# Performance work log

Hardware: AMD Instinct MI355X
Metric: run time of the kernel (lower is better)

The kernel has to match this reference:

```python
import jax, jax.numpy as jnp
import numpy as np

NUM_HEADS = 16
HEAD_DIM = 64
MAX_REL = 128
NEG_INF = -1e30


def setup_inputs() -> dict:
    key = jax.random.key(0)
    ks = jax.random.split(key, 5)
    B, L, D = 2, 2048, 1024
    x = jax.random.normal(ks[0], (B, L, D), dtype=jnp.float32)
    key_padding_mask = jnp.zeros((B, L), dtype=bool)  # True = padded
    Wqkv = jax.random.normal(ks[1], (D, 3 * D), dtype=jnp.float32) * (D ** -0.5)
    bqkv = jnp.zeros((3 * D,), dtype=jnp.float32)
    Wout = jax.random.normal(ks[2], (D, D), dtype=jnp.float32) * (D ** -0.5)
    bout = jnp.zeros((D,), dtype=jnp.float32)
    bias_table = jax.random.normal(ks[3], (2 * MAX_REL + 1, NUM_HEADS), dtype=jnp.float32) * 0.02
    return {"x": x, "key_padding_mask": key_padding_mask, "Wqkv": Wqkv,
            "bqkv": bqkv, "Wout": Wout, "bout": bout, "bias_table": bias_table}


def _rel_bias(bias_table, L):
    # relative position index: clamp(k - q, -MAX_REL, MAX_REL) + MAX_REL -> [L, L]
    rel = jnp.arange(L)[None, :] - jnp.arange(L)[:, None]
    idx = jnp.clip(rel, -MAX_REL, MAX_REL) + MAX_REL
    return bias_table[idx].transpose(2, 0, 1)  # [H, L, L]


def reference(x, key_padding_mask, Wqkv, bqkv, Wout, bout, bias_table):
    B, L, D = x.shape
    H, hd = NUM_HEADS, HEAD_DIM
    qkv = x @ Wqkv + bqkv                      # [B, L, 3D]
    q, k, v = jnp.split(qkv, 3, axis=-1)
    q = q.reshape(B, L, H, hd).transpose(0, 2, 1, 3)  # [B, H, L, hd]
    k = k.reshape(B, L, H, hd).transpose(0, 2, 1, 3)
    v = v.reshape(B, L, H, hd).transpose(0, 2, 1, 3)
    scores = jnp.einsum('bhqd,bhkd->bhqk', q, k) * (hd ** -0.5)
    scores = scores + _rel_bias(bias_table, L)[None]   # [B, H, L, L]
    scores = jnp.where(key_padding_mask[:, None, None, :], NEG_INF, scores)
    attn = jax.nn.softmax(scores, axis=-1)
    out = jnp.einsum('bhqk,bhkd->bhqd', attn, v)       # [B, H, L, hd]
    out = out.transpose(0, 2, 1, 3).reshape(B, L, D)
    return out @ Wout + bout
```

## Files before the change

kernel.cpp:

```cpp
#include <hip/hip_runtime.h>
#include <hip/hip_bf16.h>
#include <stdint.h>

#define LSEQ 2048
#define BATCH 2
#define DMODEL 1024
#define NH 16
#define HD 64

typedef __attribute__((ext_vector_type(8))) short bf16x8;
typedef __attribute__((ext_vector_type(4))) float f32x4;

__device__ __forceinline__ short f2bf(float f) {
  union { float f; uint32_t u; } v; v.f = f;
  uint32_t r = v.u + 0x8000u;
  return (short)(r >> 16);
}

__device__ __forceinline__ uint32_t pack_bf16(float lo, float hi) {
  union { float f; uint32_t u; } a, b; a.f = lo; b.f = hi;
  uint32_t al = (a.u + 0x8000u) >> 16;
  uint32_t bh = (b.u + 0x8000u) & 0xFFFF0000u;
  return al | bh;
}

__device__ __forceinline__ float exp2_fast(float x) {
#if __has_builtin(__builtin_amdgcn_exp2f)
  return __builtin_amdgcn_exp2f(x);
#else
  float r; asm("v_exp_f32 %0, %1" : "=v"(r) : "v"(x)); return r;
#endif
}

__device__ __forceinline__ void gll16(const void* g, void* l) {
  __builtin_amdgcn_global_load_lds(
      (const __attribute__((address_space(1))) void*)g,
      (__attribute__((address_space(3))) void*)l, 16, 0, 0);
}

__global__ void cvt_bf16(const float* __restrict__ in, short* __restrict__ out, int n) {
  int i = (blockIdx.x * blockDim.x + threadIdx.x) * 4;
  if (i < n) {
    float4 v = *(const float4*)(in + i);
    short4 o;
    o.x = f2bf(v.x); o.y = f2bf(v.y); o.z = f2bf(v.z); o.w = f2bf(v.w);
    *(short4*)(out + i) = o;
  }
}

__global__ void transpose_cvt(const float* __restrict__ in, short* __restrict__ out,
                              int K, int N) {
  __shared__ float tile[32][33];
  int kb = blockIdx.x * 32, nb = blockIdx.y * 32;
  int tx = threadIdx.x & 31, ty = threadIdx.x >> 5;
  #pragma unroll
  for (int i = ty; i < 32; i += 8)
    tile[i][tx] = in[(size_t)(kb + i) * N + nb + tx];
  __syncthreads();
  #pragma unroll
  for (int i = ty; i < 32; i += 8)
    out[(size_t)(nb + i) * K + kb + tx] = f2bf(tile[tx][i]);
}

template <int EPI>
__global__ __launch_bounds__(256, 2) void gemm_bt(
    const short* __restrict__ A, const short* __restrict__ Bt,
    const float* __restrict__ bias, float* __restrict__ outf,
    short* __restrict__ q_out, short* __restrict__ k_out, short* __restrict__ v_out) {
  constexpr int K = 1024, BK = 32;
  __shared__ short Als[128 * BK];
  __shared__ short Bls[128 * BK];
  const int tid = threadIdx.x;
  const int lane = tid & 63;
  const int m0 = blockIdx.x * 128;
  const int n0 = blockIdx.y * 128;
  const int wid = tid >> 6;
  const int wm = (wid >> 1) * 64, wn = (wid & 1) * 64;

  f32x4 acc[4][4] = {};

  for (int kt = 0; kt < K / BK; ++kt) {
    const int k0 = kt * BK;
    __syncthreads();
    #pragma unroll
    for (int inst = 0; inst < 2; ++inst) {
      int c = inst * 256 + tid;
      int row = c >> 2, cc = (c & 3) * 8;
      gll16(A + (size_t)(m0 + row) * K + k0 + cc, Als + c * 8);
      gll16(Bt + (size_t)(n0 + row) * K + k0 + cc, Bls + c * 8);
    }
    __syncthreads();
    bf16x8 af[4], bfv[4];
    #pragma unroll
    for (int m = 0; m < 4; ++m)
      af[m] = *(const bf16x8*)(Als + (wm + m * 16 + (lane & 15)) * BK + (lane >> 4) * 8);
    #pragma unroll
    for (int n = 0; n < 4; ++n)
      bfv[n] = *(const bf16x8*)(Bls + (wn + n * 16 + (lane & 15)) * BK + (lane >> 4) * 8);
    #pragma unroll
    for (int m = 0; m < 4; ++m)
      #pragma unroll
      for (int n = 0; n < 4; ++n)
        acc[m][n] = __builtin_amdgcn_mfma_f32_16x16x32_bf16(af[m], bfv[n], acc[m][n], 0, 0, 0);
  }

  #pragma unroll
  for (int m = 0; m < 4; ++m) {
    #pragma unroll
    for (int n = 0; n < 4; ++n) {
      #pragma unroll
      for (int r = 0; r < 4; ++r) {
        int row = m0 + wm + m * 16 + (lane >> 4) * 4 + r;
        int col = n0 + wn + n * 16 + (lane & 15);
        float val = acc[m][n][r] + bias[col];
        if (EPI == 1) {
          outf[(size_t)row * DMODEL + col] = val;
        } else {
          int b = row >> 11, l = row & 2047;
          int which = col >> 10, rem = col & 1023;
          int hn = rem >> 6, d = rem & 63;
          size_t bh = (size_t)b * NH + hn;
          if (which == 0)       q_out[(bh * LSEQ + l) * HD + d] = f2bf(val * 0.1803368801f);
          else if (which == 1)  k_out[(bh * LSEQ + l) * HD + d] = f2bf(val);
          else                  v_out[(bh * HD + d) * LSEQ + l] = f2bf(val);
        }
      }
    }
  }
}

__global__ __launch_bounds__(256, 2) void attn_kernel(
    const short* __restrict__ qb, const short* __restrict__ kb,
    const short* __restrict__ vtb, const unsigned char* __restrict__ kpm,
    const float* __restrict__ bias_table, short* __restrict__ ob) {
  constexpr int NT = LSEQ / 64;
  __shared__ short Kls[2][64 * 64];
  __shared__ short Vls[2][64 * 64];
  __shared__ short Pls[4][32 * 64];
  __shared__ float biasc[257];
  __shared__ unsigned mbits_s;

  const int tid = threadIdx.x, lane = tid & 63, wid = tid >> 6;
  const int g = lane >> 4, c = lane & 15;
  const int q0 = blockIdx.x * 128, h = blockIdx.y, b = blockIdx.z;
  const size_t bh = (size_t)b * NH + h;
  const short* qbase = qb + bh * LSEQ * HD;
  const short* kbase = kb + bh * LSEQ * HD;
  const short* vbase = vtb + bh * HD * LSEQ;
  const unsigned char* kpmb = kpm + (size_t)b * LSEQ;

  bf16x8 qf[2][2];
  #pragma unroll
  for (int qg = 0; qg < 2; ++qg)
    #pragma unroll
    for (int ks = 0; ks < 2; ++ks) {
      int qrow = q0 + wid * 32 + qg * 16 + c;
      qf[qg][ks] = *(const bf16x8*)(qbase + (size_t)qrow * HD + ks * 32 + g * 8);
    }

  if (tid < 32) {
    const uint4* mp = (const uint4*)(kpmb + tid * 64);
    uint4 m0 = mp[0], m1 = mp[1], m2 = mp[2], m3 = mp[3];
    unsigned anyb = m0.x | m0.y | m0.z | m0.w | m1.x | m1.y | m1.z | m1.w |
                    m2.x | m2.y | m2.z | m2.w | m3.x | m3.y | m3.z | m3.w;
    unsigned long long bal = __ballot(anyb != 0);
    if (tid == 0) mbits_s = (unsigned)bal;
  }
  for (int i = tid; i < 257; i += 256) biasc[i] = bias_table[i * NH + h] * 1.44269504f;
  __syncthreads();
  const unsigned mbits = mbits_s;
  const float cb_lo = biasc[0], cb_hi = biasc[256];

  auto stage = [&](int t, int bbuf) {
    const int kv0s = t * 64;
    #pragma unroll
    for (int inst = 0; inst < 2; ++inst) {
      int cc0 = inst * 256 + tid;
      int row = cc0 >> 3, cc = cc0 & 7;
      int scc = cc ^ (row & 7);
      gll16(kbase + (size_t)(kv0s + row) * HD + scc * 8, &Kls[bbuf][cc0 * 8]);
      gll16(vbase + (size_t)row * LSEQ + kv0s + scc * 8, &Vls[bbuf][cc0 * 8]);
    }
  };

  f32x4 o[4][2], l_acc[2];
  #pragma unroll
  for (int nt = 0; nt < 4; ++nt)
    #pragma unroll
    for (int qg = 0; qg < 2; ++qg) o[nt][qg] = (f32x4){0.f, 0.f, 0.f, 0.f};
  l_acc[0] = (f32x4){0.f, 0.f, 0.f, 0.f};
  l_acc[1] = (f32x4){0.f, 0.f, 0.f, 0.f};

  bf16x8 onesf;
  #pragma unroll
  for (int j = 0; j < 8; ++j) onesf[j] = (short)0x3F80;

  char* pw = (char*)&Pls[wid][0];
  const int c7s = (c & 7) << 4;

  stage(0, 0);

  for (int t = 0; t < NT; ++t) {
    const int bb = t & 1;
    const int kv0 = t * 64;
    if (t < NT - 1) {
      stage(t + 1, bb ^ 1);
      asm volatile("s_waitcnt vmcnt(4) lgkmcnt(0)" ::: "memory");
    } else {
      asm volatile("s_waitcnt vmcnt(0) lgkmcnt(0)" ::: "memory");
    }
    __builtin_amdgcn_s_barrier();
    __builtin_amdgcn_sched_barrier(0);

    f32x4 st[4][2];
    #pragma unroll
    for (int nt = 0; nt < 4; ++nt) {
      f32x4 a0 = {}, a1 = {};
      #pragma unroll
      for (int ks = 0; ks < 2; ++ks) {
        int krow = nt * 16 + c;
        int kbyte = ks * 64 + g * 16;
        const bf16x8 kf =
            *(const bf16x8*)((const char*)&Kls[bb][0] + krow * 128 + (kbyte ^ c7s));
        a0 = __builtin_amdgcn_mfma_f32_16x16x32_bf16(kf, qf[0][ks], a0, 0, 0, 0);
        a1 = __builtin_amdgcn_mfma_f32_16x16x32_bf16(kf, qf[1][ks], a1, 0, 0, 0);
      }
      st[nt][0] = a0; st[nt][1] = a1;
    }

    const int dw = kv0 - q0 - wid * 32;
    if (dw >= 160 || dw <= -192) {
      const float cb = dw > 0 ? cb_hi : cb_lo;
      #pragma unroll
      for (int nt = 0; nt < 4; ++nt)
        #pragma unroll
        for (int qg = 0; qg < 2; ++qg)
          #pragma unroll
          for (int r = 0; r < 4; ++r) st[nt][qg][r] += cb;
    } else {
      #pragma unroll
      for (int nt = 0; nt < 4; ++nt)
        #pragma unroll
        for (int qg = 0; qg < 2; ++qg) {
          const int base = dw + nt * 16 + g * 4 - qg * 16 - c;
          #pragma unroll
          for (int r = 0; r < 4; ++r) {
            int rel = base + r;
            rel = rel < -128 ? -128 : (rel > 128 ? 128 : rel);
            st[nt][qg][r] += biasc[rel + 128];
          }
        }
    }
    if (mbits & (1u << t)) {
      #pragma unroll
      for (int nt = 0; nt < 4; ++nt)
        #pragma unroll
        for (int r = 0; r < 4; ++r) {
          float mk = kpmb[kv0 + nt * 16 + g * 4 + r] ? -1e30f : 0.f;
          st[nt][0][r] += mk;
          st[nt][1][r] += mk;
        }
    }

    #pragma unroll
    for (int qg = 0; qg < 2; ++qg)
      #pragma unroll
      for (int nt = 0; nt < 4; ++nt) {
        uint32_t p01 = pack_bf16(exp2_fast(st[nt][qg][0]), exp2_fast(st[nt][qg][1]));
        uint32_t p23 = pack_bf16(exp2_fast(st[nt][qg][2]), exp2_fast(st[nt][qg][3]));
        uint2 w; w.x = p01; w.y = p23;
        *(uint2*)(pw + (qg * 16 + c) * 128 + ((nt * 32 + g * 8) ^ c7s)) = w;
      }

    asm volatile("s_waitcnt lgkmcnt(0)" ::: "memory");
    __builtin_amdgcn_sched_barrier(0);

    #pragma unroll
    for (int ks = 0; ks < 2; ++ks) {
      const int pbyte = ks * 64 + g * 16;
      bf16x8 pa0 = *(const bf16x8*)(pw + c * 128 + (pbyte ^ c7s));
      bf16x8 pa1 = *(const bf16x8*)(pw + (16 + c) * 128 + (pbyte ^ c7s));
      l_acc[0] = __builtin_amdgcn_mfma_f32_16x16x32_bf16(pa0, onesf, l_acc[0], 0, 0, 0);
      l_acc[1] = __builtin_amdgcn_mfma_f32_16x16x32_bf16(pa1, onesf, l_acc[1], 0, 0, 0);
      #pragma unroll
      for (int nt = 0; nt < 4; ++nt) {
        int vrow = nt * 16 + c;
        const bf16x8 vf =
            *(const bf16x8*)((const char*)&Vls[bb][0] + vrow * 128 + (pbyte ^ c7s));
        o[nt][0] = __builtin_amdgcn_mfma_f32_16x16x32_bf16(pa0, vf, o[nt][0], 0, 0, 0);
        o[nt][1] = __builtin_amdgcn_mfma_f32_16x16x32_bf16(pa1, vf, o[nt][1], 0, 0, 0);
      }
    }

    __builtin_amdgcn_sched_barrier(0);
    __builtin_amdgcn_s_barrier();
  }

  #pragma unroll
  for (int qg = 0; qg < 2; ++qg)
    #pragma unroll
    for (int r = 0; r < 4; ++r) {
      float inv = 1.f / l_acc[qg][r];
      int qrow = q0 + wid * 32 + qg * 16 + g * 4 + r;
      size_t obase = ((size_t)b * LSEQ + qrow) * DMODEL + (size_t)h * HD;
      #pragma unroll
      for (int nt = 0; nt < 4; ++nt)
        ob[obase + nt * 16 + c] = f2bf(o[nt][qg][r] * inv);
    }
}

extern "C" void kernel_launch(void* const* d_in, const int* in_sizes, int n_in,
                              void* d_out, int out_size, void* d_ws, size_t ws_size,
                              hipStream_t stream) {
  (void)in_sizes; (void)n_in; (void)out_size; (void)ws_size;
  const float* x = (const float*)d_in[0];
  const unsigned char* kpm = (const unsigned char*)d_in[1];
  const float* Wqkv = (const float*)d_in[2];
  const float* bqkv = (const float*)d_in[3];
  const float* Wout = (const float*)d_in[4];
  const float* bout = (const float*)d_in[5];
  const float* btab = (const float*)d_in[6];
  float* out = (float*)d_out;

  short* ws = (short*)d_ws;
  short* xbf   = ws;
  short* wqkvT = xbf + 4194304;
  short* woutT = wqkvT + 3145728;
  short* qbuf  = woutT + 1048576;
  short* kbuf  = qbuf + 4194304;
  short* vtbuf = kbuf + 4194304;
  short* obuf  = vtbuf + 4194304;

  cvt_bf16<<<dim3(4096), dim3(256), 0, stream>>>(x, xbf, 4194304);
  transpose_cvt<<<dim3(32, 96), dim3(256), 0, stream>>>(Wqkv, wqkvT, 1024, 3072);
  transpose_cvt<<<dim3(32, 32), dim3(256), 0, stream>>>(Wout, woutT, 1024, 1024);

  gemm_bt<0><<<dim3(32, 24), dim3(256), 0, stream>>>(xbf, wqkvT, bqkv, nullptr,
                                                     qbuf, kbuf, vtbuf);
  attn_kernel<<<dim3(16, 16, 2), dim3(256), 0, stream>>>(qbuf, kbuf, vtbuf, kpm, btab, obuf);
  gemm_bt<1><<<dim3(32, 8), dim3(256), 0, stream>>>(obuf, woutT, bout, out,
                                                    nullptr, nullptr, nullptr);
}
```

Before: 137.6 us.

## Double-buffer GEMM LDS tiles with async prefetch and swizzle attention block order

```diff
diff --git a/kernel.cpp b/kernel.cpp
--- a/kernel.cpp
+++ b/kernel.cpp
@@ -63,13 +63,13 @@
 }
 
 template <int EPI>
-__global__ __launch_bounds__(256, 2) void gemm_bt(
+__global__ __launch_bounds__(256, 3) void gemm_bt(
     const short* __restrict__ A, const short* __restrict__ Bt,
     const float* __restrict__ bias, float* __restrict__ outf,
     short* __restrict__ q_out, short* __restrict__ k_out, short* __restrict__ v_out) {
-  constexpr int K = 1024, BK = 32;
-  __shared__ short Als[128 * BK];
-  __shared__ short Bls[128 * BK];
+  constexpr int K = 1024, BK = 32, NKT = K / BK;
+  __shared__ short Als[2][128 * BK];
+  __shared__ short Bls[2][128 * BK];
   const int tid = threadIdx.x;
   const int lane = tid & 63;
   const int m0 = blockIdx.x * 128;
@@ -79,29 +79,45 @@
 
   f32x4 acc[4][4] = {};
 
-  for (int kt = 0; kt < K / BK; ++kt) {
+  auto stage = [&](int kt, int bbuf) {
     const int k0 = kt * BK;
-    __syncthreads();
     #pragma unroll
     for (int inst = 0; inst < 2; ++inst) {
       int c = inst * 256 + tid;
       int row = c >> 2, cc = (c & 3) * 8;
-      gll16(A + (size_t)(m0 + row) * K + k0 + cc, Als + c * 8);
-      gll16(Bt + (size_t)(n0 + row) * K + k0 + cc, Bls + c * 8);
-    }
-    __syncthreads();
+      gll16(A + (size_t)(m0 + row) * K + k0 + cc, &Als[bbuf][c * 8]);
+      gll16(Bt + (size_t)(n0 + row) * K + k0 + cc, &Bls[bbuf][c * 8]);
+    }
+  };
+
+  stage(0, 0);
+
+  for (int kt = 0; kt < NKT; ++kt) {
+    const int bb = kt & 1;
+    if (kt < NKT - 1) {
+      stage(kt + 1, bb ^ 1);
+      asm volatile("s_waitcnt vmcnt(4)" ::: "memory");
+    } else {
+      asm volatile("s_waitcnt vmcnt(0)" ::: "memory");
+    }
+    __builtin_amdgcn_s_barrier();
+    __builtin_amdgcn_sched_barrier(0);
+
     bf16x8 af[4], bfv[4];
     #pragma unroll
     for (int m = 0; m < 4; ++m)
-      af[m] = *(const bf16x8*)(Als + (wm + m * 16 + (lane & 15)) * BK + (lane >> 4) * 8);
+      af[m] = *(const bf16x8*)(&Als[bb][0] + (wm + m * 16 + (lane & 15)) * BK + (lane >> 4) * 8);
     #pragma unroll
     for (int n = 0; n < 4; ++n)
-      bfv[n] = *(const bf16x8*)(Bls + (wn + n * 16 + (lane & 15)) * BK + (lane >> 4) * 8);
+      bfv[n] = *(const bf16x8*)(&Bls[bb][0] + (wn + n * 16 + (lane & 15)) * BK + (lane >> 4) * 8);
     #pragma unroll
     for (int m = 0; m < 4; ++m)
       #pragma unroll
       for (int n = 0; n < 4; ++n)
         acc[m][n] = __builtin_amdgcn_mfma_f32_16x16x32_bf16(af[m], bfv[n], acc[m][n], 0, 0, 0);
+
+    __builtin_amdgcn_sched_barrier(0);
+    __builtin_amdgcn_s_barrier();
   }
 
   #pragma unroll
@@ -142,7 +158,11 @@
 
   const int tid = threadIdx.x, lane = tid & 63, wid = tid >> 6;
   const int g = lane >> 4, c = lane & 15;
-  const int q0 = blockIdx.x * 128, h = blockIdx.y, b = blockIdx.z;
+  const int lin = blockIdx.x;
+  const int swz = (lin & 7) * 64 + (lin >> 3);
+  const int q0 = (swz & 15) * 128;
+  const int h = (swz >> 4) & 15;
+  const int b = swz >> 8;
   const size_t bh = (size_t)b * NH + h;
   const short* qbase = qb + bh * LSEQ * HD;
   const short* kbase = kb + bh * LSEQ * HD;
@@ -337,7 +357,7 @@
 
   gemm_bt<0><<<dim3(32, 24), dim3(256), 0, stream>>>(xbf, wqkvT, bqkv, nullptr,
                                                      qbuf, kbuf, vtbuf);
-  attn_kernel<<<dim3(16, 16, 2), dim3(256), 0, stream>>>(qbuf, kbuf, vtbuf, kpm, btab, obuf);
+  attn_kernel<<<dim3(512), dim3(256), 0, stream>>>(qbuf, kbuf, vtbuf, kpm, btab, obuf);
   gemm_bt<1><<<dim3(32, 8), dim3(256), 0, stream>>>(obuf, woutT, bout, out,
                                                     nullptr, nullptr, nullptr);
 }
```

Result: no change. 136.0 us (-1.2%).
